# Kernel tuning notes

Hardware: AMD Instinct MI355X
Metric: run time of the kernel (lower is better)

The kernel has to match this reference:

```python
import jax, jax.numpy as jnp
import numpy as np

N = 10000      # nodes
E = 160000     # edges (avg degree 16)
DIN = 512      # in_channels
H = 512        # hidden_channels
OUT = 128      # out_channels
L = 3          # num_layers
EPS_LN = 1e-5


def _ln(x):
    # F.layer_norm over last dim, no learned affine
    m = jnp.mean(x, axis=-1, keepdims=True)
    v = jnp.mean((x - m) ** 2, axis=-1, keepdims=True)
    return (x - m) * jax.lax.rsqrt(v + EPS_LN)


def setup_inputs() -> dict:
    key = jax.random.key(0)
    ks = jax.random.split(key, 16)
    s = 0.02
    return {
        "x": jax.random.normal(ks[0], (N, DIN), jnp.float32),
        "edge_index": jax.random.randint(ks[1], (2, E), 0, N, dtype=jnp.int64),
        "W_in": jax.random.normal(ks[2], (DIN, H), jnp.float32) * s,
        "b_in": jnp.zeros((H,), jnp.float32),
        "Wq": jax.random.normal(ks[3], (L, H, H), jnp.float32) * s,
        "Wk": jax.random.normal(ks[4], (L, H, H), jnp.float32) * s,
        "Wv": jax.random.normal(ks[5], (L, H, H), jnp.float32) * s,
        "Wo": jax.random.normal(ks[6], (L, H, H), jnp.float32) * s,
        "bo": jnp.zeros((L, H), jnp.float32),
        "W_gcn": jax.random.normal(ks[7], (H, H), jnp.float32) * s,
        "b_gcn": jnp.zeros((H,), jnp.float32),
        "W_mix": jax.random.normal(ks[8], (2 * H, H), jnp.float32) * s,
        "b_mix": jnp.zeros((H,), jnp.float32),
        "W_cls": jax.random.normal(ks[9], (H, OUT), jnp.float32) * s,
        "b_cls": jnp.zeros((OUT,), jnp.float32),
    }


def _attn_layer(x, wq, wk, wv, wo, bo):
    q = jax.nn.elu(x @ wq) + 1.0               # [N,H], positive feature map
    k = jax.nn.elu(x @ wk) + 1.0               # [N,H]
    v = x @ wv                                  # [N,H]
    kv = k.T @ v                                # [H,H]
    z = 1.0 / jnp.maximum(q @ k.sum(axis=0), 1e-6)   # [N]
    h = (q @ kv) * z[:, None]                   # [N,H]
    return h @ wo + bo


def _gcn(x, edge_index, w, b):
    # PyG GCNConv: x@W, add self-loops, symmetric D^-1/2 (A+I) D^-1/2, +bias
    xw = x @ w
    n = xw.shape[0]
    loops = jnp.arange(n, dtype=edge_index.dtype)
    src = jnp.concatenate([edge_index[0], loops])
    dst = jnp.concatenate([edge_index[1], loops])
    deg = jax.ops.segment_sum(jnp.ones_like(dst, jnp.float32), dst, num_segments=n)
    dis = jnp.where(deg > 0, jax.lax.rsqrt(jnp.maximum(deg, 1e-12)), 0.0)
    norm = dis[src] * dis[dst]                  # [E+N]
    msg = xw[src] * norm[:, None]               # [E+N,H]
    return jax.ops.segment_sum(msg, dst, num_segments=n) + b


def reference(x, edge_index, W_in, b_in, Wq, Wk, Wv, Wo, bo,
              W_gcn, b_gcn, W_mix, b_mix, W_cls, b_cls):
    # eval mode: dropout is identity
    x0 = jax.nn.relu(x @ W_in + b_in)           # [N,H]
    h_global = x0
    for i in range(Wq.shape[0]):
        h = _attn_layer(h_global, Wq[i], Wk[i], Wv[i], Wo[i], bo[i])
        h_global = _ln(h_global + h)
    h_graph = jax.nn.relu(_gcn(x0, edge_index, W_gcn, b_gcn))
    h = jax.nn.relu(jnp.concatenate([h_global, h_graph], axis=-1) @ W_mix + b_mix)
    return h @ W_cls + b_cls                    # [N,OUT]
```

## Files before the change

### kernel.cpp

```cpp
#include <hip/hip_runtime.h>
#include <hip/hip_bf16.h>

#define NNODES 10000
#define EEDGES 160000
#define HD     512
#define OUTD   128
#define NLAYERS 3
#define MP     10112
#define KTP    10240

#define ACT_NONE 0
#define ACT_RELU 1
#define ACT_ELU1 2

typedef __attribute__((ext_vector_type(8))) short bf16x8;
typedef __attribute__((ext_vector_type(4))) float f32x4;

__device__ __forceinline__ void gload16(const void* g, void* l) {
  __builtin_amdgcn_global_load_lds(
      (const __attribute__((address_space(1))) void*)g,
      (__attribute__((address_space(3))) void*)l, 16, 0, 0);
}

__device__ __forceinline__ void unp8(uint4 v, float* f) {
  const ushort* u = (const ushort*)&v;
#pragma unroll
  for (int j = 0; j < 8; ++j) f[j] = __uint_as_float(((unsigned)u[j]) << 16);
}

__device__ __forceinline__ ushort f2bu(float f) {
  __hip_bfloat16 h = __float2bfloat16(f);
  return *reinterpret_cast<ushort*>(&h);
}

__device__ __forceinline__ float elu1f(float v) {
  return (v > 0.f) ? (v + 1.0f) : __expf(v);
}

#define INIT_N (3 * HD * HD + NNODES + 1 + 512 * 120 * 2)
#define B0 ((INIT_N + 255) / 256)
#define B1 ((int)((long)MP * HD / 8 / 256))
#define B2 (17 * 256)
__global__ __launch_bounds__(256) void setup_k(
    int* cnt, int* flag, float* kvf, __hip_bfloat16* kT, __hip_bfloat16* vT,
    const float* x, __hip_bfloat16* xb,
    const float* W_in, const float* Wq, const float* Wk, const float* Wv,
    const float* Wo, const float* W_gcn, const float* W_mix, const float* W_cls,
    __hip_bfloat16* WT, __hip_bfloat16* WMT, __hip_bfloat16* WCT)
{
  __shared__ float t[32][33];
  int b = blockIdx.x;
  if (b < B0) {
    int i = b * 256 + threadIdx.x;
    if (i < 3 * HD * HD) { kvf[i] = 0.f; return; }
    i -= 3 * HD * HD;
    if (i < NNODES) { cnt[i] = 0; return; }
    i -= NNODES;
    if (i == 0) { *flag = 0; return; }
    i -= 1;
    if (i < 512 * 120 * 2) {
      int bb = i / (512 * 120);
      int r = (i % (512 * 120)) / 120;
      int c = (i % 120);
      uint* T = (uint*)(bb == 0 ? kT : vT);
      T[((long)r * KTP + NNODES) / 2 + c] = 0u;
    }
    return;
  }
  b -= B0;
  if (b < B1) {
    long i = (long)b * 256 + threadIdx.x;
    long base = i * 8;
    int row = (int)(base >> 9);
    ushort o[8];
    if (row < NNODES) {
      float4 a = *(const float4*)(x + base);
      float4 c = *(const float4*)(x + base + 4);
      float f[8] = {a.x, a.y, a.z, a.w, c.x, c.y, c.z, c.w};
#pragma unroll
      for (int j = 0; j < 8; ++j) o[j] = f2bu(f[j]);
    } else {
#pragma unroll
      for (int j = 0; j < 8; ++j) o[j] = 0;
    }
    *(uint4*)((ushort*)xb + base) = *(const uint4*)o;
    return;
  }
  b -= B1;
  int z = b >> 8;
  int rem = b & 255;
  int by = rem >> 4, bx = rem & 15;
  const float* src;
  __hip_bfloat16* out;
  int ldout = 512, koff = 0, ldsrc = 512;
  if (z == 0) { src = W_in; out = WT; }
  else if (z <= 9) {
    int l = (z - 1) / 3, w = (z - 1) % 3;
    src = (w == 0 ? Wq : w == 1 ? Wk : Wv) + (long)l * 262144;
    out = WT + (long)z * 262144;
  } else if (z <= 12) { src = Wo + (long)(z - 10) * 262144; out = WT + (long)z * 262144; }
  else if (z == 13) { src = W_gcn; out = WT + 13L * 262144; }
  else if (z <= 15) { src = W_mix + (long)(z - 14) * 262144; out = WMT; ldout = 1024; koff = (z - 14) * 512; }
  else {
    if (bx >= 4) return;
    src = W_cls; out = WCT; ldsrc = 128;
  }
  int r0 = by * 32, c0 = bx * 32;
  int tx = threadIdx.x & 31, ty = threadIdx.x >> 5;
#pragma unroll
  for (int i = 0; i < 32; i += 8) t[ty + i][tx] = src[(long)(r0 + ty + i) * ldsrc + c0 + tx];
  __syncthreads();
#pragma unroll
  for (int i = 0; i < 32; i += 8)
    out[(long)(c0 + ty + i) * ldout + koff + r0 + tx] = __float2bfloat16(t[tx][ty + i]);
}

__global__ void probe_i64_k(const void* ei, int* flag, int E_) {
  int i = blockIdx.x * blockDim.x + threadIdx.x;
  bool nz = (i < E_) && (((const int*)ei)[2 * i + 1] != 0);
  unsigned long long m = __ballot(nz);
  if ((threadIdx.x & 63) == 0 && m) atomicOr(flag, 1);
}
__device__ inline void load_edge(const void* ei, int is_i32, int e, int E_, int& s, int& d) {
  if (is_i32) { s = ((const int*)ei)[e]; d = ((const int*)ei)[E_ + e]; }
  else { s = (int)((const long long*)ei)[e]; d = (int)((const long long*)ei)[E_ + e]; }
}

template<int ACT, int HAS_BIAS, int HAS_SCALE, int OUTF, int OUTB, int ATOMIC, int TQKV, int KSUM>
__global__ __launch_bounds__(256) void mgemm(
    const __hip_bfloat16* __restrict__ A, const __hip_bfloat16* __restrict__ Bt,
    const float* __restrict__ bias, const float* __restrict__ rowscale,
    float* __restrict__ Cf, __hip_bfloat16* __restrict__ Cb,
    __hip_bfloat16* __restrict__ kTp, __hip_bfloat16* __restrict__ vTp,
    float* __restrict__ aux,
    int M, int lda, int ldb, int ldc, int ldcb, int Ksz)
{
  if (KSUM) {
    if (blockIdx.z >= 16) {
      int role = (blockIdx.z - 16) * 16 + blockIdx.y * 4 + blockIdx.x;
      int wv = threadIdx.x >> 6, lane = threadIdx.x & 63;
#pragma unroll
      for (int rr = 0; rr < 4; ++rr) {
        int i = role * 16 + wv * 4 + rr;
        const ushort* kr = (const ushort*)A + (long)i * lda;
        float s = 0.f;
        for (int off = lane * 8; off < NNODES; off += 512) {
          uint4 v = *(const uint4*)(kr + off);
          float f[8]; unp8(v, f);
#pragma unroll
          for (int j = 0; j < 8; ++j) s += f[j];
        }
#pragma unroll
        for (int o = 32; o > 0; o >>= 1) s += __shfl_down(s, o);
        if (lane == 0) aux[i] = s;
      }
      return;
    }
  }
  __shared__ __align__(16) char smem[TQKV ? 35072 : 32768];

  int nwg = gridDim.x * gridDim.y;
  int orig = blockIdx.y * gridDim.x + blockIdx.x;
  int qq = nwg >> 3, rr8 = nwg & 7;
  int xcd = orig & 7, idx = orig >> 3;
  int wg = (xcd < rr8 ? xcd * (qq + 1) : rr8 * (qq + 1) + (xcd - rr8) * qq) + idx;
  int bx = wg % gridDim.x, by = wg / gridDim.x;

  int tid = threadIdx.x;
  int lane = tid & 63;
  int wave = tid >> 6;
  int wm = wave >> 1, wn = wave & 1;
  int row0 = by * 128;
  int col0 = bx * 128;
  int koff = blockIdx.z * Ksz;
  int srow8 = lane >> 3;
  int sb = ((lane & 7) * 16) ^ (srow8 << 4);

  f32x4 acc[4][4];
#pragma unroll
  for (int i = 0; i < 4; ++i)
#pragma unroll
    for (int j = 0; j < 4; ++j) acc[i][j] = f32x4{0.f, 0.f, 0.f, 0.f};

  int r16 = lane & 15;
  int kg = (lane >> 4) * 16;
  int rsw = (r16 & 7) << 4;

  for (int k0 = koff; k0 < koff + Ksz; k0 += 64) {
#pragma unroll
    for (int j = 0; j < 4; ++j) {
      int rbase = wave * 32 + j * 8;
      const char* ga = (const char*)(A + (long)(row0 + rbase + srow8) * lda + k0) + sb;
      gload16(ga, smem + rbase * 128);
      const char* gb = (const char*)(Bt + (long)(col0 + rbase + srow8) * ldb + k0) + sb;
      gload16(gb, smem + 16384 + rbase * 128);
    }
    __syncthreads();
#pragma unroll
    for (int s = 0; s < 2; ++s) {
      bf16x8 af[4], bfr[4];
      int off = ((s * 64 + kg) ^ rsw);
#pragma unroll
      for (int i = 0; i < 4; ++i)
        af[i] = *(const bf16x8*)(smem + (wm * 64 + i * 16 + r16) * 128 + off);
#pragma unroll
      for (int i = 0; i < 4; ++i)
        bfr[i] = *(const bf16x8*)(smem + 16384 + (wn * 64 + i * 16 + r16) * 128 + off);
#pragma unroll
      for (int i = 0; i < 4; ++i)
#pragma unroll
        for (int j = 0; j < 4; ++j)
          acc[i][j] = __builtin_amdgcn_mfma_f32_16x16x32_bf16(af[i], bfr[j], acc[i][j], 0, 0, 0);
    }
    __syncthreads();
  }

  int rg = (lane >> 4) * 4;
  if (TQKV) {
    ushort* eps = (ushort*)smem;
    int colg = col0 + wn * 64;
    int g = colg >> 9;
    int cbase = col0 & 511;
#pragma unroll
    for (int i = 0; i < 4; ++i) {
#pragma unroll
      for (int j = 0; j < 4; ++j) {
        int c_l = wn * 64 + j * 16 + r16;
        int row_l = wm * 64 + i * 16 + rg;
        if (g == 0) {
#pragma unroll
          for (int r = 0; r < 4; ++r)
            eps[(row_l + r) * 136 + c_l] = f2bu(elu1f(acc[i][j][r]));
        } else {
          ushort4 o;
          o.x = f2bu(g == 1 ? elu1f(acc[i][j][0]) : acc[i][j][0]);
          o.y = f2bu(g == 1 ? elu1f(acc[i][j][1]) : acc[i][j][1]);
          o.z = f2bu(g == 1 ? elu1f(acc[i][j][2]) : acc[i][j][2]);
          o.w = f2bu(g == 1 ? elu1f(acc[i][j][3]) : acc[i][j][3]);
          *(ushort4*)&eps[c_l * 136 + row_l] = o;
        }
      }
    }
    __syncthreads();
    int l16 = tid & 15, cw = tid >> 4;
    if (g == 0) {
#pragma unroll
      for (int rr = cw; rr < 128; rr += 16) {
        int node = row0 + rr;
        if (node < NNODES)
          *(uint4*)((ushort*)Cb + (long)node * ldcb + cbase + l16 * 8) =
              *(const uint4*)&eps[rr * 136 + l16 * 8];
      }
    } else {
      ushort* T = (ushort*)(g == 1 ? kTp : vTp);
      int node0 = row0 + l16 * 8;
      if (node0 < NNODES) {
#pragma unroll
        for (int cc = cw; cc < 128; cc += 16)
          *(uint4*)(T + (long)(cbase + cc) * KTP + node0) = *(const uint4*)&eps[cc * 136 + l16 * 8];
      }
    }
    return;
  }
#pragma unroll
  for (int i = 0; i < 4; ++i) {
#pragma unroll
    for (int j = 0; j < 4; ++j) {
      int col = col0 + wn * 64 + j * 16 + r16;
#pragma unroll
      for (int r = 0; r < 4; ++r) {
        int row = row0 + wm * 64 + i * 16 + rg + r;
        if (row >= M) continue;
        float v = acc[i][j][r];
        if (ATOMIC) { atomicAdd(&Cf[(long)row * ldc + col], v); continue; }
        if (HAS_SCALE) v *= rowscale[row];
        if (HAS_BIAS) v += bias[col];
        if (ACT == ACT_RELU) v = fmaxf(v, 0.f);
        if (ACT == ACT_ELU1) v = elu1f(v);
        if (OUTF) Cf[(long)row * ldc + col] = v;
        if (OUTB) Cb[(long)row * ldcb + col] = __float2bfloat16(v);
      }
    }
  }
}

__global__ __launch_bounds__(256) void cast_z_k(
    const float* __restrict__ kvf, __hip_bfloat16* __restrict__ kvb,
    const __hip_bfloat16* __restrict__ qb, const float* __restrict__ ksum,
    float* __restrict__ z)
{
  int b = blockIdx.x;
  if (b < 128) {
    int i = b * 256 + threadIdx.x;
    float4 a = ((const float4*)kvf)[2 * i], c = ((const float4*)kvf)[2 * i + 1];
    float f[8] = {a.x, a.y, a.z, a.w, c.x, c.y, c.z, c.w};
    ushort o[8];
#pragma unroll
    for (int j = 0; j < 8; ++j) o[j] = f2bu(f[j]);
    *(uint4*)((ushort*)kvb + (long)i * 8) = *(const uint4*)o;
    return;
  }
  long gid = (long)(b - 128) * 256 + threadIdx.x;
  int row = (int)(gid >> 6), lane = (int)(gid & 63);
  if (row >= NNODES) return;
  uint4 qv = *(const uint4*)((const ushort*)qb + (long)row * HD + lane * 8);
  float f[8]; unp8(qv, f);
  const float* kk = ksum + lane * 8;
  float s = 0.f;
#pragma unroll
  for (int j = 0; j < 8; ++j) s += f[j] * kk[j];
#pragma unroll
  for (int o = 32; o > 0; o >>= 1) s += __shfl_down(s, o);
  if (lane == 0) z[row] = 1.0f / fmaxf(s, 1e-6f);
}

__global__ __launch_bounds__(256) void ln_res_k(float* __restrict__ hg,
                                                const __hip_bfloat16* __restrict__ hb,
                                                __hip_bfloat16* __restrict__ hgcat) {
  int wid = (blockIdx.x * 256 + threadIdx.x) >> 6;
  int lane = threadIdx.x & 63;
  if (wid >= NNODES) return;
  float* row = hg + (long)wid * HD + lane * 8;
  uint4 hv = *(const uint4*)((const ushort*)hb + (long)wid * HD + lane * 8);
  float hf[8]; unp8(hv, hf);
  float4 p0 = *(const float4*)row, p1 = *(const float4*)(row + 4);
  float a[8] = {p0.x + hf[0], p0.y + hf[1], p0.z + hf[2], p0.w + hf[3],
                p1.x + hf[4], p1.y + hf[5], p1.z + hf[6], p1.w + hf[7]};
  float s = 0.f;
#pragma unroll
  for (int j = 0; j < 8; ++j) s += a[j];
#pragma unroll
  for (int o = 1; o < 64; o <<= 1) s += __shfl_xor(s, o);
  float mean = s * (1.0f / HD);
  float vs = 0.f;
#pragma unroll
  for (int j = 0; j < 8; ++j) { a[j] -= mean; vs += a[j] * a[j]; }
#pragma unroll
  for (int o = 1; o < 64; o <<= 1) vs += __shfl_xor(vs, o);
  float inv = rsqrtf(vs * (1.0f / HD) + 1e-5f);
  ushort ob[8];
#pragma unroll
  for (int j = 0; j < 8; ++j) { a[j] *= inv; ob[j] = f2bu(a[j]); }
  *(float4*)row = make_float4(a[0], a[1], a[2], a[3]);
  *(float4*)(row + 4) = make_float4(a[4], a[5], a[6], a[7]);
  *(uint4*)((ushort*)hgcat + (long)wid * 1024 + lane * 8) = *(const uint4*)ob;
}

__global__ void cnt_k(const void* ei, const int* flag, int* cnt, int E_) {
  int e = blockIdx.x * blockDim.x + threadIdx.x;
  if (e >= E_) return;
  int s, d; load_edge(ei, *flag, e, E_, s, d);
  atomicAdd(&cnt[d], 1);
}
__global__ __launch_bounds__(256) void scan_k(const int* __restrict__ cnt, int* __restrict__ rowptr,
                                              int* __restrict__ cursor, float* __restrict__ dis) {
  __shared__ int ps[256];
  int t = threadIdx.x;
  int lo = t * 40, hi = min(lo + 40, NNODES);
  int s = 0;
  for (int i = lo; i < hi; ++i) s += cnt[i];
  ps[t] = s;
  __syncthreads();
  for (int o = 1; o < 256; o <<= 1) {
    int v = (t >= o) ? ps[t - o] : 0;
    __syncthreads();
    ps[t] += v;
    __syncthreads();
  }
  int run = (t == 0) ? 0 : ps[t - 1];
  for (int i = lo; i < hi; ++i) {
    rowptr[i] = run; cursor[i] = run;
    dis[i] = rsqrtf((float)cnt[i] + 1.0f);
    run += cnt[i];
  }
  if (t == 255) rowptr[NNODES] = run;
}
__global__ void csrfill_k(const void* ei, const int* flag, int* cursor, int* csr, int E_) {
  int e = blockIdx.x * blockDim.x + threadIdx.x;
  if (e >= E_) return;
  int s, d; load_edge(ei, *flag, e, E_, s, d);
  int pos = atomicAdd(&cursor[d], 1);
  csr[pos] = s;
}
__global__ __launch_bounds__(256) void gcn_gather_k(
    const __hip_bfloat16* __restrict__ xwb, const int* __restrict__ rowptr,
    const int* __restrict__ csr, const float* __restrict__ dis,
    const float* __restrict__ bgcn, __hip_bfloat16* __restrict__ hgcat)
{
  int wid = (blockIdx.x * 256 + threadIdx.x) >> 6;
  int lane = threadIdx.x & 63;
  if (wid >= NNODES) return;
  int d = wid;
  float dd = dis[d];
  float acc[8], f[8], f2[8];
  uint4 v = *(const uint4*)((const ushort*)xwb + (long)d * HD + lane * 8);
  unp8(v, f);
#pragma unroll
  for (int j = 0; j < 8; ++j) acc[j] = f[j] * dd * dd;
  int e0 = rowptr[d], e1 = rowptr[d + 1];
  int e = e0;
  for (; e + 1 < e1; e += 2) {
    int s0 = csr[e], s1 = csr[e + 1];
    float w0 = dis[s0] * dd, w1 = dis[s1] * dd;
    uint4 xv0 = *(const uint4*)((const ushort*)xwb + (long)s0 * HD + lane * 8);
    uint4 xv1 = *(const uint4*)((const ushort*)xwb + (long)s1 * HD + lane * 8);
    unp8(xv0, f); unp8(xv1, f2);
#pragma unroll
    for (int j = 0; j < 8; ++j) acc[j] = fmaf(f[j], w0, fmaf(f2[j], w1, acc[j]));
  }
  if (e < e1) {
    int sN = csr[e];
    float w = dis[sN] * dd;
    uint4 xv = *(const uint4*)((const ushort*)xwb + (long)sN * HD + lane * 8);
    unp8(xv, f);
#pragma unroll
    for (int j = 0; j < 8; ++j) acc[j] = fmaf(f[j], w, acc[j]);
  }
  const float* bb = bgcn + lane * 8;
  ushort o[8];
#pragma unroll
  for (int j = 0; j < 8; ++j) o[j] = f2bu(fmaxf(acc[j] + bb[j], 0.f));
  *(uint4*)((ushort*)hgcat + (long)d * 1024 + 512 + lane * 8) = *(const uint4*)o;
}

extern "C" void kernel_launch(void* const* d_in, const int* in_sizes, int n_in,
                              void* d_out, int out_size, void* d_ws, size_t ws_size,
                              hipStream_t stream) {
  const float* x     = (const float*)d_in[0];
  const void*  ei    = d_in[1];
  const float* W_in  = (const float*)d_in[2];
  const float* b_in  = (const float*)d_in[3];
  const float* Wq    = (const float*)d_in[4];
  const float* Wk    = (const float*)d_in[5];
  const float* Wv    = (const float*)d_in[6];
  const float* Wo    = (const float*)d_in[7];
  const float* bo    = (const float*)d_in[8];
  const float* W_gcn = (const float*)d_in[9];
  const float* b_gcn = (const float*)d_in[10];
  const float* W_mix = (const float*)d_in[11];
  const float* b_mix = (const float*)d_in[12];
  const float* W_cls = (const float*)d_in[13];
  const float* b_cls = (const float*)d_in[14];
  float* out = (float*)d_out;

  char* p = (char*)d_ws;
  __hip_bfloat16* WT  = (__hip_bfloat16*)p; p += 14L * 262144 * 2;
  __hip_bfloat16* WMT = (__hip_bfloat16*)p; p += 512L * 1024 * 2;
  __hip_bfloat16* WCT = (__hip_bfloat16*)p; p += 128L * 512 * 2;
  float* hg = (float*)p; p += (long)MP * HD * 4;
  __hip_bfloat16* hgcat = (__hip_bfloat16*)p; p += (long)MP * 1024 * 2;
  __hip_bfloat16* qb = (__hip_bfloat16*)p; p += (long)MP * HD * 2;
  __hip_bfloat16* vT = (__hip_bfloat16*)p; p += 512L * KTP * 2;
  __hip_bfloat16* kT = (__hip_bfloat16*)p; p += 512L * KTP * 2;
  float* kvf = (float*)p; p += 3L * 512 * 512 * 4;
  __hip_bfloat16* kvb  = (__hip_bfloat16*)p; p += 512L * 512 * 2;
  __hip_bfloat16* kvoT = (__hip_bfloat16*)p; p += 512L * 512 * 2;
  float* ksum = (float*)p; p += 3L * 512 * 4;
  float* zb   = (float*)p; p += (long)MP * 4;
  int* cnt    = (int*)p; p += 40000;
  int* rowptr = (int*)p; p += 40016;
  int* cursor = (int*)p; p += 40000;
  float* dis  = (float*)p; p += 40000;
  int* csr    = (int*)p; p += 640000;
  int* flag   = (int*)p; p += 4;

  __hip_bfloat16* xb    = qb;
  __hip_bfloat16* xwb   = qb;
  __hip_bfloat16* hb    = kT;
  __hip_bfloat16* hmixb = kT;

  dim3 blk(256);
  dim3 gG(4, MP / 128);
  dim3 gQKV(12, MP / 128);
  dim3 gKV(4, 4, 18);
  dim3 gS(4, 4);
  dim3 gCls(1, MP / 128);

  setup_k<<<B0 + B1 + B2, blk, 0, stream>>>(cnt, flag, kvf, kT, vT, x, xb,
                                            W_in, Wq, Wk, Wv, Wo, W_gcn, W_mix, W_cls,
                                            WT, WMT, WCT);
  probe_i64_k<<<(EEDGES + 255) / 256, 256, 0, stream>>>(ei, flag, EEDGES);

  mgemm<ACT_RELU, 1, 0, 1, 1, 0, 0, 0><<<gG, blk, 0, stream>>>(
      xb, WT, b_in, nullptr, hg, hgcat, nullptr, nullptr, nullptr,
      NNODES, HD, HD, HD, 1024, HD);

  mgemm<ACT_NONE, 0, 0, 0, 1, 0, 0, 0><<<gG, blk, 0, stream>>>(
      hgcat, WT + 13L * 262144, nullptr, nullptr, nullptr, xwb, nullptr, nullptr, nullptr,
      NNODES, 1024, HD, HD, HD, HD);
  cnt_k<<<(EEDGES + 255) / 256, 256, 0, stream>>>(ei, flag, cnt, EEDGES);
  scan_k<<<1, 256, 0, stream>>>(cnt, rowptr, cursor, dis);
  csrfill_k<<<(EEDGES + 255) / 256, 256, 0, stream>>>(ei, flag, cursor, csr, EEDGES);
  gcn_gather_k<<<2500, blk, 0, stream>>>(xwb, rowptr, csr, dis, b_gcn, hgcat);

  for (int l = 0; l < NLAYERS; ++l) {
    const __hip_bfloat16* BtQKV = WT + (long)(1 + 3 * l) * 262144;
    const __hip_bfloat16* WoT   = WT + (long)(10 + l) * 262144;
    float* kvfl  = kvf + (long)l * HD * HD;
    float* ksuml = ksum + (long)l * HD;

    mgemm<ACT_NONE, 0, 0, 0, 0, 0, 1, 0><<<gQKV, blk, 0, stream>>>(
        hgcat, BtQKV, nullptr, nullptr, nullptr, qb, kT, vT, nullptr,
        NNODES, 1024, HD, HD, HD, HD);

    mgemm<ACT_NONE, 0, 0, 0, 0, 1, 0, 1><<<gKV, blk, 0, stream>>>(
        kT, vT, nullptr, nullptr, kvfl, nullptr, nullptr, nullptr, ksuml,
        HD, KTP, KTP, HD, HD, 640);

    cast_z_k<<<2628, blk, 0, stream>>>(kvfl, kvb, qb, ksuml, zb);

    mgemm<ACT_NONE, 0, 0, 0, 1, 0, 0, 0><<<gS, blk, 0, stream>>>(
        WoT, kvb, nullptr, nullptr, nullptr, kvoT, nullptr, nullptr, nullptr,
        HD, HD, HD, HD, HD, HD);

    mgemm<ACT_NONE, 1, 1, 0, 1, 0, 0, 0><<<gG, blk, 0, stream>>>(
        qb, kvoT, bo + (long)l * HD, zb, nullptr, hb, nullptr, nullptr, nullptr,
        NNODES, HD, HD, HD, HD, HD);
    ln_res_k<<<2500, blk, 0, stream>>>(hg, hb, hgcat);
  }

  mgemm<ACT_RELU, 1, 0, 0, 1, 0, 0, 0><<<gG, blk, 0, stream>>>(
      hgcat, WMT, b_mix, nullptr, nullptr, hmixb, nullptr, nullptr, nullptr,
      NNODES, 1024, 1024, HD, HD, 1024);
  mgemm<ACT_NONE, 1, 0, 1, 0, 0, 0, 0><<<gCls, blk, 0, stream>>>(
      hmixb, WCT, b_cls, nullptr, out, nullptr, nullptr, nullptr, nullptr,
      NNODES, HD, HD, OUTD, OUTD, HD);
}
```

Baseline: 664.8 us.

## Replace atomic split-K kv GEMM with partial buffers and small-tile kernel

The k^T v split-K GEMM used to accumulate into a zeroed fp32 buffer with atomicAdd. It now writes 16 separate partial slices, which cast_z_k sums before converting to bf16. The same new 64x64-tile kernel also handles the small Wo*kv GEMM, giving that step 64 blocks instead of 16. The kv buffer no longer needs zeroing in setup, but the partial buffers add extra memory traffic (16x512x512 fp32 written and read each layer).

Result: faster. 610.0 us (-8.2%).

```diff
diff --git a/kernel.cpp b/kernel.cpp
--- a/kernel.cpp
+++ b/kernel.cpp
@@ -37,12 +37,12 @@
   return (v > 0.f) ? (v + 1.0f) : __expf(v);
 }
 
-#define INIT_N (3 * HD * HD + NNODES + 1 + 512 * 120 * 2)
+#define INIT_N (NNODES + 1 + 512 * 120 * 2)
 #define B0 ((INIT_N + 255) / 256)
 #define B1 ((int)((long)MP * HD / 8 / 256))
 #define B2 (17 * 256)
 __global__ __launch_bounds__(256) void setup_k(
-    int* cnt, int* flag, float* kvf, __hip_bfloat16* kT, __hip_bfloat16* vT,
+    int* cnt, int* flag, __hip_bfloat16* kT, __hip_bfloat16* vT,
     const float* x, __hip_bfloat16* xb,
     const float* W_in, const float* Wq, const float* Wk, const float* Wv,
     const float* Wo, const float* W_gcn, const float* W_mix, const float* W_cls,
@@ -52,8 +52,6 @@
   int b = blockIdx.x;
   if (b < B0) {
     int i = b * 256 + threadIdx.x;
-    if (i < 3 * HD * HD) { kvf[i] = 0.f; return; }
-    i -= 3 * HD * HD;
     if (i < NNODES) { cnt[i] = 0; return; }
     i -= NNODES;
     if (i == 0) { *flag = 0; return; }
@@ -126,37 +124,14 @@
   else { s = (int)((const long long*)ei)[e]; d = (int)((const long long*)ei)[E_ + e]; }
 }
 
-template<int ACT, int HAS_BIAS, int HAS_SCALE, int OUTF, int OUTB, int ATOMIC, int TQKV, int KSUM>
+template<int ACT, int HAS_BIAS, int HAS_SCALE, int OUTF, int OUTB, int TQKV>
 __global__ __launch_bounds__(256) void mgemm(
     const __hip_bfloat16* __restrict__ A, const __hip_bfloat16* __restrict__ Bt,
     const float* __restrict__ bias, const float* __restrict__ rowscale,
     float* __restrict__ Cf, __hip_bfloat16* __restrict__ Cb,
     __hip_bfloat16* __restrict__ kTp, __hip_bfloat16* __restrict__ vTp,
-    float* __restrict__ aux,
     int M, int lda, int ldb, int ldc, int ldcb, int Ksz)
 {
-  if (KSUM) {
-    if (blockIdx.z >= 16) {
-      int role = (blockIdx.z - 16) * 16 + blockIdx.y * 4 + blockIdx.x;
-      int wv = threadIdx.x >> 6, lane = threadIdx.x & 63;
-#pragma unroll
-      for (int rr = 0; rr < 4; ++rr) {
-        int i = role * 16 + wv * 4 + rr;
-        const ushort* kr = (const ushort*)A + (long)i * lda;
-        float s = 0.f;
-        for (int off = lane * 8; off < NNODES; off += 512) {
-          uint4 v = *(const uint4*)(kr + off);
-          float f[8]; unp8(v, f);
-#pragma unroll
-          for (int j = 0; j < 8; ++j) s += f[j];
-        }
-#pragma unroll
-        for (int o = 32; o > 0; o >>= 1) s += __shfl_down(s, o);
-        if (lane == 0) aux[i] = s;
-      }
-      return;
-    }
-  }
   __shared__ __align__(16) char smem[TQKV ? 35072 : 32768];
 
   int nwg = gridDim.x * gridDim.y;
@@ -272,7 +247,6 @@
         int row = row0 + wm * 64 + i * 16 + rg + r;
         if (row >= M) continue;
         float v = acc[i][j][r];
-        if (ATOMIC) { atomicAdd(&Cf[(long)row * ldc + col], v); continue; }
         if (HAS_SCALE) v *= rowscale[row];
         if (HAS_BIAS) v += bias[col];
         if (ACT == ACT_RELU) v = fmaxf(v, 0.f);
@@ -284,20 +258,113 @@
   }
 }
 
+template<int KSUM, int OUTB>
+__global__ __launch_bounds__(256) void kvgemm_k(
+    const __hip_bfloat16* __restrict__ A, const __hip_bfloat16* __restrict__ Bt,
+    float* __restrict__ Cf, __hip_bfloat16* __restrict__ Cb,
+    float* __restrict__ aux, int lda, int ldb, int Ksz)
+{
+  int lane = threadIdx.x & 63;
+  int wave = threadIdx.x >> 6;
+  if (KSUM && blockIdx.z == gridDim.z - 1) {
+    int bi = blockIdx.y * 8 + blockIdx.x;
+#pragma unroll
+    for (int rr = 0; rr < 2; ++rr) {
+      int i = bi * 8 + wave * 2 + rr;
+      const ushort* kr = (const ushort*)A + (long)i * lda;
+      float s = 0.f;
+      for (int off = lane * 8; off < NNODES; off += 512) {
+        uint4 v = *(const uint4*)(kr + off);
+        float f[8]; unp8(v, f);
+#pragma unroll
+        for (int j = 0; j < 8; ++j) s += f[j];
+      }
+#pragma unroll
+      for (int o = 32; o > 0; o >>= 1) s += __shfl_down(s, o);
+      if (lane == 0) aux[i] = s;
+    }
+    return;
+  }
+  __shared__ __align__(16) char smem[16384];
+  int wm = wave >> 1, wn = wave & 1;
+  int i0 = blockIdx.y * 64, j0 = blockIdx.x * 64;
+  int koff = blockIdx.z * Ksz;
+  int srow8 = lane >> 3;
+  int sb = ((lane & 7) * 16) ^ (srow8 << 4);
+  f32x4 acc[2][2];
+#pragma unroll
+  for (int i = 0; i < 2; ++i)
+#pragma unroll
+    for (int j = 0; j < 2; ++j) acc[i][j] = f32x4{0.f, 0.f, 0.f, 0.f};
+  int r16 = lane & 15;
+  int kg = (lane >> 4) * 16;
+  int rsw = (r16 & 7) << 4;
+
+  for (int k0 = koff; k0 < koff + Ksz; k0 += 64) {
+#pragma unroll
+    for (int j = 0; j < 2; ++j) {
+      int rbase = wave * 16 + j * 8;
+      const char* ga = (const char*)(A + (long)(i0 + rbase + srow8) * lda + k0) + sb;
+      gload16(ga, smem + rbase * 128);
+      const char* gb = (const char*)(Bt + (long)(j0 + rbase + srow8) * ldb + k0) + sb;
+      gload16(gb, smem + 8192 + rbase * 128);
+    }
+    __syncthreads();
+#pragma unroll
+    for (int s = 0; s < 2; ++s) {
+      bf16x8 af[2], bfr[2];
+      int off = ((s * 64 + kg) ^ rsw);
+#pragma unroll
+      for (int i = 0; i < 2; ++i)
+        af[i] = *(const bf16x8*)(smem + (wm * 32 + i * 16 + r16) * 128 + off);
+#pragma unroll
+      for (int i = 0; i < 2; ++i)
+        bfr[i] = *(const bf16x8*)(smem + 8192 + (wn * 32 + i * 16 + r16) * 128 + off);
+#pragma unroll
+      for (int i = 0; i < 2; ++i)
+#pragma unroll
+        for (int j = 0; j < 2; ++j)
+          acc[i][j] = __builtin_amdgcn_mfma_f32_16x16x32_bf16(af[i], bfr[j], acc[i][j], 0, 0, 0);
+    }
+    __syncthreads();
+  }
+  int rg = (lane >> 4) * 4;
+  float* Cp = Cf + (long)blockIdx.z * 262144;
+#pragma unroll
+  for (int i = 0; i < 2; ++i) {
+#pragma unroll
+    for (int j = 0; j < 2; ++j) {
+      int col = j0 + wn * 32 + j * 16 + r16;
+#pragma unroll
+      for (int r = 0; r < 4; ++r) {
+        int row = i0 + wm * 32 + i * 16 + rg + r;
+        if (OUTB) Cb[(long)row * 512 + col] = __float2bfloat16(acc[i][j][r]);
+        else Cp[(long)row * 512 + col] = acc[i][j][r];
+      }
+    }
+  }
+}
+
 __global__ __launch_bounds__(256) void cast_z_k(
-    const float* __restrict__ kvf, __hip_bfloat16* __restrict__ kvb,
+    const float* __restrict__ kvp, __hip_bfloat16* __restrict__ kvb,
     const __hip_bfloat16* __restrict__ qb, const float* __restrict__ ksum,
     float* __restrict__ z)
 {
   int b = blockIdx.x;
   if (b < 128) {
-    int i = b * 256 + threadIdx.x;
-    float4 a = ((const float4*)kvf)[2 * i], c = ((const float4*)kvf)[2 * i + 1];
-    float f[8] = {a.x, a.y, a.z, a.w, c.x, c.y, c.z, c.w};
+    long i = (long)b * 256 + threadIdx.x;
+    float acc8[8] = {};
+#pragma unroll
+    for (int s = 0; s < 16; ++s) {
+      const float* sp = kvp + (long)s * 262144 + i * 8;
+      float4 a = *(const float4*)sp, c = *(const float4*)(sp + 4);
+      acc8[0] += a.x; acc8[1] += a.y; acc8[2] += a.z; acc8[3] += a.w;
+      acc8[4] += c.x; acc8[5] += c.y; acc8[6] += c.z; acc8[7] += c.w;
+    }
     ushort o[8];
 #pragma unroll
-    for (int j = 0; j < 8; ++j) o[j] = f2bu(f[j]);
-    *(uint4*)((ushort*)kvb + (long)i * 8) = *(const uint4*)o;
+    for (int j = 0; j < 8; ++j) o[j] = f2bu(acc8[j]);
+    *(uint4*)((ushort*)kvb + i * 8) = *(const uint4*)o;
     return;
   }
   long gid = (long)(b - 128) * 256 + threadIdx.x;
@@ -452,10 +519,10 @@
   __hip_bfloat16* qb = (__hip_bfloat16*)p; p += (long)MP * HD * 2;
   __hip_bfloat16* vT = (__hip_bfloat16*)p; p += 512L * KTP * 2;
   __hip_bfloat16* kT = (__hip_bfloat16*)p; p += 512L * KTP * 2;
-  float* kvf = (float*)p; p += 3L * 512 * 512 * 4;
+  float* kvp = (float*)p; p += 16L * 512 * 512 * 4;
   __hip_bfloat16* kvb  = (__hip_bfloat16*)p; p += 512L * 512 * 2;
   __hip_bfloat16* kvoT = (__hip_bfloat16*)p; p += 512L * 512 * 2;
-  float* ksum = (float*)p; p += 3L * 512 * 4;
+  float* ksum = (float*)p; p += 512 * 4;
   float* zb   = (float*)p; p += (long)MP * 4;
   int* cnt    = (int*)p; p += 40000;
   int* rowptr = (int*)p; p += 40016;
@@ -472,21 +539,21 @@
   dim3 blk(256);
   dim3 gG(4, MP / 128);
   dim3 gQKV(12, MP / 128);
-  dim3 gKV(4, 4, 18);
-  dim3 gS(4, 4);
+  dim3 gKV(8, 8, 17);
+  dim3 gS(8, 8, 1);
   dim3 gCls(1, MP / 128);
 
-  setup_k<<<B0 + B1 + B2, blk, 0, stream>>>(cnt, flag, kvf, kT, vT, x, xb,
+  setup_k<<<B0 + B1 + B2, blk, 0, stream>>>(cnt, flag, kT, vT, x, xb,
                                             W_in, Wq, Wk, Wv, Wo, W_gcn, W_mix, W_cls,
                                             WT, WMT, WCT);
   probe_i64_k<<<(EEDGES + 255) / 256, 256, 0, stream>>>(ei, flag, EEDGES);
 
-  mgemm<ACT_RELU, 1, 0, 1, 1, 0, 0, 0><<<gG, blk, 0, stream>>>(
-      xb, WT, b_in, nullptr, hg, hgcat, nullptr, nullptr, nullptr,
+  mgemm<ACT_RELU, 1, 0, 1, 1, 0><<<gG, blk, 0, stream>>>(
+      xb, WT, b_in, nullptr, hg, hgcat, nullptr, nullptr,
       NNODES, HD, HD, HD, 1024, HD);
 
-  mgemm<ACT_NONE, 0, 0, 0, 1, 0, 0, 0><<<gG, blk, 0, stream>>>(
-      hgcat, WT + 13L * 262144, nullptr, nullptr, nullptr, xwb, nullptr, nullptr, nullptr,
+  mgemm<ACT_NONE, 0, 0, 0, 1, 0><<<gG, blk, 0, stream>>>(
+      hgcat, WT + 13L * 262144, nullptr, nullptr, nullptr, xwb, nullptr, nullptr,
       NNODES, 1024, HD, HD, HD, HD);
   cnt_k<<<(EEDGES + 255) / 256, 256, 0, stream>>>(ei, flag, cnt, EEDGES);
   scan_k<<<1, 256, 0, stream>>>(cnt, rowptr, cursor, dis);
@@ -496,33 +563,27 @@
   for (int l = 0; l < NLAYERS; ++l) {
     const __hip_bfloat16* BtQKV = WT + (long)(1 + 3 * l) * 262144;
     const __hip_bfloat16* WoT   = WT + (long)(10 + l) * 262144;
-    float* kvfl  = kvf + (long)l * HD * HD;
-    float* ksuml = ksum + (long)l * HD;
-
-    mgemm<ACT_NONE, 0, 0, 0, 0, 0, 1, 0><<<gQKV, blk, 0, stream>>>(
-        hgcat, BtQKV, nullptr, nullptr, nullptr, qb, kT, vT, nullptr,
+
+    mgemm<ACT_NONE, 0, 0, 0, 0, 1><<<gQKV, blk, 0, stream>>>(
+        hgcat, BtQKV, nullptr, nullptr, nullptr, qb, kT, vT,
         NNODES, 1024, HD, HD, HD, HD);
 
-    mgemm<ACT_NONE, 0, 0, 0, 0, 1, 0, 1><<<gKV, blk, 0, stream>>>(
-        kT, vT, nullptr, nullptr, kvfl, nullptr, nullptr, nullptr, ksuml,
-        HD, KTP, KTP, HD, HD, 640);
-
-    cast_z_k<<<2628, blk, 0, stream>>>(kvfl, kvb, qb, ksuml, zb);
-
-    mgemm<ACT_NONE, 0, 0, 0, 1, 0, 0, 0><<<gS, blk, 0, stream>>>(
-        WoT, kvb, nullptr, nullptr, nullptr, kvoT, nullptr, nullptr, nullptr,
-        HD, HD, HD, HD, HD, HD);
-
-    mgemm<ACT_NONE, 1, 1, 0, 1, 0, 0, 0><<<gG, blk, 0, stream>>>(
-        qb, kvoT, bo + (long)l * HD, zb, nullptr, hb, nullptr, nullptr, nullptr,
+    kvgemm_k<1, 0><<<gKV, blk, 0, stream>>>(kT, vT, kvp, nullptr, ksum, KTP, KTP, 640);
+
+    cast_z_k<<<2628, blk, 0, stream>>>(kvp, kvb, qb, ksum, zb);
+
+    kvgemm_k<0, 1><<<gS, blk, 0, stream>>>(WoT, kvb, nullptr, kvoT, nullptr, 512, 512, 512);
+
+    mgemm<ACT_NONE, 1, 1, 0, 1, 0><<<gG, blk, 0, stream>>>(
+        qb, kvoT, bo + (long)l * HD, zb, nullptr, hb, nullptr, nullptr,
         NNODES, HD, HD, HD, HD, HD);
     ln_res_k<<<2500, blk, 0, stream>>>(hg, hb, hgcat);
   }
 
-  mgemm<ACT_RELU, 1, 0, 0, 1, 0, 0, 0><<<gG, blk, 0, stream>>>(
-      hgcat, WMT, b_mix, nullptr, nullptr, hmixb, nullptr, nullptr, nullptr,
+  mgemm<ACT_RELU, 1, 0, 0, 1, 0><<<gG, blk, 0, stream>>>(
+      hgcat, WMT, b_mix, nullptr, nullptr, hmixb, nullptr, nullptr,
       NNODES, 1024, 1024, HD, HD, 1024);
-  mgemm<ACT_NONE, 1, 0, 1, 0, 0, 0, 0><<<gCls, blk, 0, stream>>>(
-      hmixb, WCT, b_cls, nullptr, out, nullptr, nullptr, nullptr, nullptr,
+  mgemm<ACT_NONE, 1, 0, 1, 0, 0><<<gCls, blk, 0, stream>>>(
+      hmixb, WCT, b_cls, nullptr, out, nullptr, nullptr, nullptr,
       NNODES, HD, HD, OUTD, OUTD, HD);
 }
```
